# Optimization experiments

Hardware: AMD Instinct MI355X
Metric: run time of the kernel (lower is better)

## Reference

```python
import jax, jax.numpy as jnp
import numpy as np
import math

B, T, C = 4, 2048, 1024
N_HEAD = 16
HEAD_DIM = C // N_HEAD


def setup_inputs() -> dict:
    key = jax.random.key(0)
    k1, k2, k3, k4, k5 = jax.random.split(key, 5)
    s = 1.0 / math.sqrt(C)
    return {
        "x": jax.random.normal(k1, (B, T, C), dtype=jnp.float32),
        "W_attn": jax.random.normal(k2, (3 * C, C), dtype=jnp.float32) * s,
        "b_attn": jax.random.normal(k3, (3 * C,), dtype=jnp.float32) * 0.02,
        "W_proj": jax.random.normal(k4, (C, C), dtype=jnp.float32) * s,
        "b_proj": jax.random.normal(k5, (C,), dtype=jnp.float32) * 0.02,
    }


def reference(x, W_attn, b_attn, W_proj, b_proj):
    Bx, Tx, Cx = x.shape
    # QKV projection (torch Linear: x @ W.T + b), split into q,k,v
    qkv = jnp.einsum("btc,dc->btd", x, W_attn) + b_attn  # [B,T,3C]
    q, k, v = jnp.split(qkv, 3, axis=-1)
    # [B,T,C] -> [B,H,T,hd]
    def to_heads(t):
        return t.reshape(Bx, Tx, N_HEAD, HEAD_DIM).transpose(0, 2, 1, 3)
    q, k, v = to_heads(q), to_heads(k), to_heads(v)
    scale = 1.0 / math.sqrt(HEAD_DIM)
    att = jnp.einsum("bhqd,bhkd->bhqk", q, k) * scale  # [B,H,T,T]
    causal = jnp.tril(jnp.ones((Tx, Tx), dtype=bool))
    att = jnp.where(causal, att, -jnp.inf)
    att = jax.nn.softmax(att, axis=-1)
    y = jnp.einsum("bhqk,bhkd->bhqd", att, v)  # [B,H,T,hd]
    y = y.transpose(0, 2, 1, 3).reshape(Bx, Tx, Cx)
    y = jnp.einsum("btc,dc->btd", y, W_proj) + b_proj
    return y
```

## Files before the change

kernel.cpp:

```cpp
#include <hip/hip_runtime.h>
#include <hip/hip_bf16.h>
#include <stdint.h>

typedef unsigned short u16;
typedef __attribute__((ext_vector_type(8))) short bf16x8;
typedef __attribute__((ext_vector_type(4))) short s16x4;
typedef __attribute__((ext_vector_type(4))) float f32x4;

#define B_SZ 4
#define T_SZ 2048
#define C_SZ 1024
#define NH   16
#define HD   64
#define LOG2E 1.44269504088896340736f

__device__ __forceinline__ u16 f2bf(float f) {
  unsigned int u = __float_as_uint(f);
  u += 0x7fffu + ((u >> 16) & 1u);
  return (u16)(u >> 16);
}
__device__ __forceinline__ u16 f2bf_hu(float f) {
  return (u16)((__float_as_uint(f) + 0x8000u) >> 16);
}
__device__ __forceinline__ void gload_lds16(const u16* g, u16* l) {
  __builtin_amdgcn_global_load_lds((const __attribute__((address_space(1))) void*)g,
                                   (__attribute__((address_space(3))) void*)l, 16, 0, 0);
}

__global__ void cast_f32_bf16(const float* __restrict__ in, u16* __restrict__ out, int n8) {
  int i = blockIdx.x * blockDim.x + threadIdx.x;
  if (i < n8) {
    const float4* p = (const float4*)in + (size_t)i * 2;
    float4 a = p[0], b = p[1];
    bf16x8 o;
    o[0] = (short)f2bf(a.x); o[1] = (short)f2bf(a.y);
    o[2] = (short)f2bf(a.z); o[3] = (short)f2bf(a.w);
    o[4] = (short)f2bf(b.x); o[5] = (short)f2bf(b.y);
    o[6] = (short)f2bf(b.z); o[7] = (short)f2bf(b.w);
    ((bf16x8*)out)[i] = o;
  }
}

template <int MODE>
__launch_bounds__(256, 3)
__global__ void gemm_bt(const u16* __restrict__ A, const u16* __restrict__ Bw,
                        const float* __restrict__ bias,
                        void* __restrict__ O0, void* __restrict__ O1, void* __restrict__ O2,
                        int M, int N, int K) {
  __shared__ __align__(16) u16 As[128 * 32];
  __shared__ __align__(16) u16 Bs[128 * 32];
  const int tid = threadIdx.x;
  const int lane = tid & 63;
  const int w = tid >> 6;
  const int wr = w >> 1, wc = w & 1;
  const int quad = lane >> 4, l16 = lane & 15;
  const int m0 = blockIdx.y * 128;
  const int n0 = blockIdx.x * 128;

  const int srow = lane >> 2;
  const int scol = (lane & 3) * 8;
  const u16* gA = A + (size_t)(m0 + w * 32 + srow) * K + scol;
  const u16* gB = Bw + (size_t)(n0 + w * 32 + srow) * K + scol;
  u16* lA0 = &As[(w * 32) * 32];
  u16* lA1 = &As[(w * 32 + 16) * 32];
  u16* lB0 = &Bs[(w * 32) * 32];
  u16* lB1 = &Bs[(w * 32 + 16) * 32];
  const size_t rstep = (size_t)16 * K;

  f32x4 acc[4][4];
#pragma unroll
  for (int i = 0; i < 4; i++)
#pragma unroll
    for (int j = 0; j < 4; j++) acc[i][j] = (f32x4){0.f, 0.f, 0.f, 0.f};

  for (int k0 = 0; k0 < K; k0 += 32) {
    __syncthreads();
    gload_lds16(gA + k0, lA0);
    gload_lds16(gA + rstep + k0, lA1);
    gload_lds16(gB + k0, lB0);
    gload_lds16(gB + rstep + k0, lB1);
    __syncthreads();
    bf16x8 af[4], bfr[4];
#pragma unroll
    for (int mt = 0; mt < 4; mt++)
      af[mt] = *(const bf16x8*)&As[(wr * 64 + mt * 16 + l16) * 32 + quad * 8];
#pragma unroll
    for (int nt = 0; nt < 4; nt++)
      bfr[nt] = *(const bf16x8*)&Bs[(wc * 64 + nt * 16 + l16) * 32 + quad * 8];
#pragma unroll
    for (int mt = 0; mt < 4; mt++)
#pragma unroll
      for (int nt = 0; nt < 4; nt++)
        acc[mt][nt] = __builtin_amdgcn_mfma_f32_16x16x32_bf16(af[mt], bfr[nt], acc[mt][nt], 0, 0, 0);
  }

  float bv[4];
#pragma unroll
  for (int nt = 0; nt < 4; nt++) bv[nt] = bias[n0 + wc * 64 + nt * 16 + l16];

  if (MODE == 0) {
    float* Cout = (float*)O0;
#pragma unroll
    for (int mt = 0; mt < 4; mt++) {
      const int row = m0 + wr * 64 + mt * 16 + quad * 4;
#pragma unroll
      for (int nt = 0; nt < 4; nt++) {
        const int col = n0 + wc * 64 + nt * 16 + l16;
#pragma unroll
        for (int r = 0; r < 4; r++)
          Cout[(size_t)(row + r) * N + col] = acc[mt][nt][r] + bv[nt];
      }
    }
  } else {
    const int nsec = (n0 + wc * 64) >> 10;
    const int hh = ((n0 + wc * 64) >> 6) & 15;
    if (nsec < 2) {
      u16* dst = (u16*)(nsec == 0 ? O0 : O1);
#pragma unroll
      for (int mt = 0; mt < 4; mt++) {
        const int row = m0 + wr * 64 + mt * 16 + quad * 4;
        const int bb = row >> 11;
        const int t = row & 2047;
#pragma unroll
        for (int nt = 0; nt < 4; nt++) {
          const int dh = nt * 16 + l16;
          const size_t a = (((size_t)bb * NH + hh) * T_SZ + t) * HD + dh;
#pragma unroll
          for (int r = 0; r < 4; r++)
            dst[a + (size_t)r * HD] = f2bf(acc[mt][nt][r] + bv[nt]);
        }
      }
    } else {
      u16* vth = (u16*)O2;
#pragma unroll
      for (int mt = 0; mt < 4; mt++) {
        const int row = m0 + wr * 64 + mt * 16 + quad * 4;
        const int bb = row >> 11;
        const int t = row & 2047;
#pragma unroll
        for (int nt = 0; nt < 4; nt++) {
          const int dh = nt * 16 + l16;
          s16x4 pk;
#pragma unroll
          for (int r = 0; r < 4; r++) pk[r] = (short)f2bf(acc[mt][nt][r] + bv[nt]);
          *(s16x4*)&vth[(((size_t)bb * NH + hh) * HD + dh) * T_SZ + t] = pk;
        }
      }
    }
  }
}

__device__ __forceinline__ void attn_step(
    int kb, int kbn, int w, int quad, int l16, int qt128, int sw0, int sw1,
    const u16* gK0, const u16* gK1, const u16* gV0, const u16* gV1,
    u16* KsF, u16* VsF, u16* PsW,
    const bf16x8 (&qf)[2][2], f32x4 (&o)[2][4], float (&l_i)[2][4]) {
  __syncthreads();

  if (kb + 1 < kbn) {
    const int nb = (kb + 1) & 1;
    const size_t ko = (size_t)(kb + 1) * 64 * HD;
    const int vo = (kb + 1) * 64;
    gload_lds16(gK0 + ko, KsF + nb * 4096 + (2 * w) * 512);
    gload_lds16(gK1 + ko, KsF + nb * 4096 + (2 * w + 1) * 512);
    gload_lds16(gV0 + vo, VsF + nb * 4096 + (2 * w) * 512);
    gload_lds16(gV1 + vo, VsF + nb * 4096 + (2 * w + 1) * 512);
  }

  const u16* Kb = KsF + (kb & 1) * 4096;
  const u16* Vb = VsF + (kb & 1) * 4096;
  const int kt0 = kb * 64;
  const float SC = 0.125f * LOG2E;

#pragma unroll
  for (int m = 0; m < 2; m++) {
    const int mrow = qt128 + w * 32 + m * 16;
    const int qr = mrow + quad * 4;
    const bool diag = (kt0 + 64 > mrow);

    f32x4 s[4];
    __builtin_amdgcn_s_setprio(1);
#pragma unroll
    for (int nt = 0; nt < 4; nt++) {
      bf16x8 kf0 = *(const bf16x8*)&Kb[(nt * 16 + l16) * 64 + sw0];
      bf16x8 kf1 = *(const bf16x8*)&Kb[(nt * 16 + l16) * 64 + sw1];
      f32x4 t0 = (f32x4){0.f, 0.f, 0.f, 0.f};
      t0 = __builtin_amdgcn_mfma_f32_16x16x32_bf16(qf[m][0], kf0, t0, 0, 0, 0);
      t0 = __builtin_amdgcn_mfma_f32_16x16x32_bf16(qf[m][1], kf1, t0, 0, 0, 0);
      s[nt] = t0;
    }
    __builtin_amdgcn_s_setprio(0);

    if (diag) {
#pragma unroll
      for (int nt = 0; nt < 4; nt++) {
        const int dk = kt0 + nt * 16 + l16 - qr;
#pragma unroll
        for (int r = 0; r < 4; r++) {
          float v = (dk > r) ? -10000.f : s[nt][r] * SC;
          s[nt][r] = exp2f(v);
        }
      }
    } else {
#pragma unroll
      for (int nt = 0; nt < 4; nt++)
#pragma unroll
        for (int r = 0; r < 4; r++)
          s[nt][r] = exp2f(s[nt][r] * SC);
    }
#pragma unroll
    for (int r = 0; r < 4; r++)
      l_i[m][r] += (s[0][r] + s[1][r]) + (s[2][r] + s[3][r]);

#pragma unroll
    for (int nt = 0; nt < 4; nt++)
#pragma unroll
      for (int r = 0; r < 4; r++)
        PsW[(quad * 4 + r) * 72 + nt * 16 + l16] = f2bf_hu(s[nt][r]);
    bf16x8 p0 = *(const bf16x8*)&PsW[l16 * 72 + quad * 8];
    bf16x8 p1 = *(const bf16x8*)&PsW[l16 * 72 + 32 + quad * 8];
    __builtin_amdgcn_s_setprio(1);
#pragma unroll
    for (int nt = 0; nt < 4; nt++) {
      bf16x8 v0 = *(const bf16x8*)&Vb[(nt * 16 + l16) * 64 + sw0];
      bf16x8 v1 = *(const bf16x8*)&Vb[(nt * 16 + l16) * 64 + sw1];
      o[m][nt] = __builtin_amdgcn_mfma_f32_16x16x32_bf16(p0, v0, o[m][nt], 0, 0, 0);
      o[m][nt] = __builtin_amdgcn_mfma_f32_16x16x32_bf16(p1, v1, o[m][nt], 0, 0, 0);
    }
    __builtin_amdgcn_s_setprio(0);
  }
}

__launch_bounds__(256, 3)
__global__ void attn_fused(const u16* __restrict__ qh, const u16* __restrict__ kh,
                           const u16* __restrict__ vth, u16* __restrict__ out) {
  __shared__ __align__(16) u16 Ks[2][64 * 64];
  __shared__ __align__(16) u16 Vs[2][64 * 64];
  __shared__ __align__(16) u16 Ps[4][16 * 72];
  const int qt = 15 - blockIdx.z;
  const int h = blockIdx.x, b = blockIdx.y;
  const int tid = threadIdx.x;
  const int lane = tid & 63, w = tid >> 6;
  const int quad = lane >> 4, l16 = lane & 15;
  const size_t bh = (size_t)b * NH + h;
  const u16* Kbase = kh + bh * T_SZ * HD;
  const u16* Vbase = vth + bh * HD * T_SZ;
  const int qt128 = qt * 128;

  const int dr = lane >> 3;
  const int dc = (lane & 7) ^ dr;
  const u16* gK0 = Kbase + (size_t)(2 * w * 8 + dr) * HD + dc * 8;
  const u16* gK1 = Kbase + (size_t)((2 * w + 1) * 8 + dr) * HD + dc * 8;
  const u16* gV0 = Vbase + (size_t)(2 * w * 8 + dr) * T_SZ + dc * 8;
  const u16* gV1 = Vbase + (size_t)((2 * w + 1) * 8 + dr) * T_SZ + dc * 8;
  u16* KsF = &Ks[0][0];
  u16* VsF = &Vs[0][0];
  u16* PsW = &Ps[w][0];

  bf16x8 qf[2][2];
#pragma unroll
  for (int m = 0; m < 2; m++) {
    const int t = qt128 + w * 32 + m * 16 + l16;
    const u16* qrow = qh + (bh * T_SZ + t) * HD;
    qf[m][0] = *(const bf16x8*)(qrow + quad * 8);
    qf[m][1] = *(const bf16x8*)(qrow + 32 + quad * 8);
  }

  f32x4 o[2][4];
  float l_i[2][4];
#pragma unroll
  for (int m = 0; m < 2; m++)
#pragma unroll
    for (int i = 0; i < 4; i++) {
      o[m][i] = (f32x4){0.f, 0.f, 0.f, 0.f};
      l_i[m][i] = 0.f;
    }

  const int kbn = 2 * qt + 2;
  const int sw0 = (quad ^ (l16 & 7)) * 8;
  const int sw1 = ((4 + quad) ^ (l16 & 7)) * 8;

  gload_lds16(gK0, KsF + (2 * w) * 512);
  gload_lds16(gK1, KsF + (2 * w + 1) * 512);
  gload_lds16(gV0, VsF + (2 * w) * 512);
  gload_lds16(gV1, VsF + (2 * w + 1) * 512);

  for (int kb = 0; kb < kbn; kb++)
    attn_step(kb, kbn, w, quad, l16, qt128, sw0, sw1,
              gK0, gK1, gV0, gV1, KsF, VsF, PsW, qf, o, l_i);

#pragma unroll
  for (int m = 0; m < 2; m++)
#pragma unroll
    for (int r = 0; r < 4; r++) {
      float v = l_i[m][r];
      v += __shfl_xor(v, 1);
      v += __shfl_xor(v, 2);
      v += __shfl_xor(v, 4);
      v += __shfl_xor(v, 8);
      const float inv = 1.f / v;
      const int t = qt128 + w * 32 + m * 16 + quad * 4 + r;
      const size_t orow = ((size_t)b * T_SZ + t) * C_SZ + (size_t)h * HD;
#pragma unroll
      for (int nt = 0; nt < 4; nt++)
        out[orow + nt * 16 + l16] = f2bf(o[m][nt][r] * inv);
    }
}

extern "C" void kernel_launch(void* const* d_in, const int* in_sizes, int n_in,
                              void* d_out, int out_size, void* d_ws, size_t ws_size,
                              hipStream_t stream) {
  (void)in_sizes; (void)n_in; (void)out_size; (void)ws_size;
  const float* x      = (const float*)d_in[0];
  const float* W_attn = (const float*)d_in[1];
  const float* b_attn = (const float*)d_in[2];
  const float* W_proj = (const float*)d_in[3];
  const float* b_proj = (const float*)d_in[4];
  float* out = (float*)d_out;

  char* ws = (char*)d_ws;
  u16* xb  = (u16*)ws;  ws += (size_t)8192 * 1024 * 2;
  u16* Wab = (u16*)ws;  ws += (size_t)3072 * 1024 * 2;
  u16* Wpb = (u16*)ws;  ws += (size_t)1024 * 1024 * 2;
  u16* qhb = (u16*)ws;  ws += (size_t)8192 * 1024 * 2;
  u16* khb = (u16*)ws;  ws += (size_t)8192 * 1024 * 2;
  u16* vtb = (u16*)ws;  ws += (size_t)8192 * 1024 * 2;
  u16* aob = (u16*)ws;

  dim3 blk(256);
  cast_f32_bf16<<<(8192 * 1024 / 8 + 255) / 256, blk, 0, stream>>>(x, xb, 8192 * 1024 / 8);
  cast_f32_bf16<<<(3072 * 1024 / 8 + 255) / 256, blk, 0, stream>>>(W_attn, Wab, 3072 * 1024 / 8);
  cast_f32_bf16<<<(1024 * 1024 / 8 + 255) / 256, blk, 0, stream>>>(W_proj, Wpb, 1024 * 1024 / 8);

  gemm_bt<1><<<dim3(3072 / 128, 8192 / 128), blk, 0, stream>>>(
      xb, Wab, b_attn, qhb, khb, vtb, 8192, 3072, 1024);
  attn_fused<<<dim3(NH, B_SZ, 16), blk, 0, stream>>>(qhb, khb, vtb, aob);
  gemm_bt<0><<<dim3(1024 / 128, 8192 / 128), blk, 0, stream>>>(
      aob, Wpb, b_proj, out, nullptr, nullptr, 8192, 1024, 1024);
}
```

Baseline: 267.7 us.

## Rewrite GEMMs with double-buffered swizzled LDS, fuse casts, fold softmax scale into Q

The two GEMMs get a new kernel body with a K-tile of 64, double-buffered LDS filled by direct global-to-LDS loads, an XOR-swizzled LDS layout, workgroup index swizzling for cache locality, and a V-transpose epilogue staged through LDS so global stores are coalesced. The three cast kernels are merged into one launch. The softmax scale and log2e factor are folded into Q at the QKV epilogue. The attention step is reorganised to share K and V fragment loads across both m-subtiles and skips the fully masked last block for the first two waves. The 64KB dynamic LDS drops occupancy to 2 blocks per CU, and the early return inside a step that contains a barrier could be a synchronisation hazard.

```diff
diff --git a/kernel.cpp b/kernel.cpp
--- a/kernel.cpp
+++ b/kernel.cpp
@@ -27,125 +27,185 @@
                                    (__attribute__((address_space(3))) void*)l, 16, 0, 0);
 }
 
-__global__ void cast_f32_bf16(const float* __restrict__ in, u16* __restrict__ out, int n8) {
+__global__ void cast3_f32_bf16(const float* __restrict__ x, const float* __restrict__ wa,
+                               const float* __restrict__ wp, u16* __restrict__ xb,
+                               u16* __restrict__ wab, u16* __restrict__ wpb) {
+  const int n1 = 8192 * 1024 / 8, n2 = 3072 * 1024 / 8, n3 = 1024 * 1024 / 8;
   int i = blockIdx.x * blockDim.x + threadIdx.x;
-  if (i < n8) {
-    const float4* p = (const float4*)in + (size_t)i * 2;
-    float4 a = p[0], b = p[1];
-    bf16x8 o;
-    o[0] = (short)f2bf(a.x); o[1] = (short)f2bf(a.y);
-    o[2] = (short)f2bf(a.z); o[3] = (short)f2bf(a.w);
-    o[4] = (short)f2bf(b.x); o[5] = (short)f2bf(b.y);
-    o[6] = (short)f2bf(b.z); o[7] = (short)f2bf(b.w);
-    ((bf16x8*)out)[i] = o;
-  }
-}
-
-template <int MODE>
-__launch_bounds__(256, 3)
-__global__ void gemm_bt(const u16* __restrict__ A, const u16* __restrict__ Bw,
-                        const float* __restrict__ bias,
-                        void* __restrict__ O0, void* __restrict__ O1, void* __restrict__ O2,
-                        int M, int N, int K) {
-  __shared__ __align__(16) u16 As[128 * 32];
-  __shared__ __align__(16) u16 Bs[128 * 32];
-  const int tid = threadIdx.x;
-  const int lane = tid & 63;
-  const int w = tid >> 6;
-  const int wr = w >> 1, wc = w & 1;
-  const int quad = lane >> 4, l16 = lane & 15;
-  const int m0 = blockIdx.y * 128;
-  const int n0 = blockIdx.x * 128;
-
-  const int srow = lane >> 2;
-  const int scol = (lane & 3) * 8;
-  const u16* gA = A + (size_t)(m0 + w * 32 + srow) * K + scol;
-  const u16* gB = Bw + (size_t)(n0 + w * 32 + srow) * K + scol;
-  u16* lA0 = &As[(w * 32) * 32];
-  u16* lA1 = &As[(w * 32 + 16) * 32];
-  u16* lB0 = &Bs[(w * 32) * 32];
-  u16* lB1 = &Bs[(w * 32 + 16) * 32];
-  const size_t rstep = (size_t)16 * K;
-
-  f32x4 acc[4][4];
-#pragma unroll
-  for (int i = 0; i < 4; i++)
-#pragma unroll
-    for (int j = 0; j < 4; j++) acc[i][j] = (f32x4){0.f, 0.f, 0.f, 0.f};
-
-  for (int k0 = 0; k0 < K; k0 += 32) {
-    __syncthreads();
-    gload_lds16(gA + k0, lA0);
-    gload_lds16(gA + rstep + k0, lA1);
-    gload_lds16(gB + k0, lB0);
-    gload_lds16(gB + rstep + k0, lB1);
-    __syncthreads();
-    bf16x8 af[4], bfr[4];
-#pragma unroll
-    for (int mt = 0; mt < 4; mt++)
-      af[mt] = *(const bf16x8*)&As[(wr * 64 + mt * 16 + l16) * 32 + quad * 8];
-#pragma unroll
-    for (int nt = 0; nt < 4; nt++)
-      bfr[nt] = *(const bf16x8*)&Bs[(wc * 64 + nt * 16 + l16) * 32 + quad * 8];
-#pragma unroll
-    for (int mt = 0; mt < 4; mt++)
-#pragma unroll
-      for (int nt = 0; nt < 4; nt++)
-        acc[mt][nt] = __builtin_amdgcn_mfma_f32_16x16x32_bf16(af[mt], bfr[nt], acc[mt][nt], 0, 0, 0);
-  }
-
+  const float* in; u16* out; int idx;
+  if (i < n1)            { in = x;  out = xb;  idx = i; }
+  else if (i < n1 + n2)  { in = wa; out = wab; idx = i - n1; }
+  else if (i < n1 + n2 + n3) { in = wp; out = wpb; idx = i - n1 - n2; }
+  else return;
+  const float4* p = (const float4*)in + (size_t)idx * 2;
+  float4 a = p[0], b = p[1];
+  bf16x8 o;
+  o[0] = (short)f2bf(a.x); o[1] = (short)f2bf(a.y);
+  o[2] = (short)f2bf(a.z); o[3] = (short)f2bf(a.w);
+  o[4] = (short)f2bf(b.x); o[5] = (short)f2bf(b.y);
+  o[6] = (short)f2bf(b.z); o[7] = (short)f2bf(b.w);
+  ((bf16x8*)out)[idx] = o;
+}
+
+#define GEMM128_PROLOG(A_, B_)                                                \
+  extern __shared__ u16 lds[];                                                \
+  u16* As = lds;                                         \
+  u16* Bs = lds + 16384;                                 \
+  const int tid = threadIdx.x;                                                \
+  const int lane = tid & 63, w = tid >> 6;                                    \
+  const int wm = w >> 1, wn = w & 1;                                          \
+  const int quad = lane >> 4, l16 = lane & 15;                                \
+  const int gx = gridDim.x;                                                   \
+  const int nwg = gx * gridDim.y;                                             \
+  const int wg0 = blockIdx.y * gx + blockIdx.x;                               \
+  const int swz = (wg0 & 7) * (nwg >> 3) + (wg0 >> 3);                        \
+  const int n0 = (swz % gx) * 128;                                            \
+  const int m0 = (swz / gx) * 128;                                            \
+  const int dr8 = lane >> 3;                                                  \
+  const int dc8 = (lane & 7) ^ dr8;                                           \
+  const u16* gAL = A_ + (size_t)(m0 + w * 32 + dr8) * K + dc8 * 8;            \
+  const u16* gBL = B_ + (size_t)(n0 + w * 32 + dr8) * K + dc8 * 8;            \
+  const int NT = K >> 6;                                                      \
+  auto stageA = [&](int tile) {                                               \
+    u16* d = As + (tile & 1) * 8192 + w * 2048;                               \
+    const u16* g = gAL + (size_t)tile * 64;                                   \
+    _Pragma("unroll")                                                         \
+    for (int sg = 0; sg < 4; ++sg)                                            \
+      gload_lds16(g + (size_t)(sg * 8) * K, d + sg * 512);                    \
+  };                                                                          \
+  auto stageB = [&](int tile) {                                               \
+    u16* d = Bs + (tile & 1) * 8192 + w * 2048;                               \
+    const u16* g = gBL + (size_t)tile * 64;                                   \
+    _Pragma("unroll")                                                         \
+    for (int sg = 0; sg < 4; ++sg)                                            \
+      gload_lds16(g + (size_t)(sg * 8) * K, d + sg * 512);                    \
+  };                                                                          \
+  f32x4 acc[4][4];                                                            \
+  _Pragma("unroll")                                                           \
+  for (int i = 0; i < 4; i++)                                                 \
+    _Pragma("unroll")                                                         \
+    for (int j = 0; j < 4; j++) acc[i][j] = (f32x4){0.f, 0.f, 0.f, 0.f};      \
+  stageA(0); stageB(0);                                                       \
+  asm volatile("s_waitcnt vmcnt(0)" ::: "memory");                            \
+  __builtin_amdgcn_s_barrier();                                               \
+  const int sK0 = ((quad) ^ (l16 & 7)) * 8;                                   \
+  const int sK1 = ((4 + quad) ^ (l16 & 7)) * 8;                               \
+  for (int tile = 0; tile < NT; ++tile) {                                     \
+    const u16* Ab = As + (tile & 1) * 8192;                                   \
+    const u16* Bb = Bs + (tile & 1) * 8192;                                   \
+    _Pragma("unroll")                                                         \
+    for (int mp = 0; mp < 2; ++mp) {                                          \
+      bf16x8 af[2][2], bfr[4][2];                                             \
+      _Pragma("unroll")                                                       \
+      for (int a = 0; a < 2; ++a) {                                           \
+        const int ro = (wm * 64 + (mp * 2 + a) * 16 + l16) * 64;              \
+        af[a][0] = *(const bf16x8*)&Ab[ro + sK0];                             \
+        af[a][1] = *(const bf16x8*)&Ab[ro + sK1];                             \
+      }                                                                       \
+      _Pragma("unroll")                                                       \
+      for (int nt = 0; nt < 4; ++nt) {                                        \
+        const int ro = (wn * 64 + nt * 16 + l16) * 64;                        \
+        bfr[nt][0] = *(const bf16x8*)&Bb[ro + sK0];                           \
+        bfr[nt][1] = *(const bf16x8*)&Bb[ro + sK1];                           \
+      }                                                                       \
+      if (mp == 0 && tile + 1 < NT) { stageA(tile + 1); stageB(tile + 1); }   \
+      asm volatile("s_waitcnt lgkmcnt(8)");                                   \
+      asm volatile("" ::: "memory");                                          \
+      __builtin_amdgcn_s_barrier();                                           \
+      asm volatile("s_waitcnt lgkmcnt(0)" ::: "memory");                      \
+      __builtin_amdgcn_sched_barrier(0);                                      \
+      __builtin_amdgcn_s_setprio(1);                                          \
+      _Pragma("unroll")                                                       \
+      for (int a = 0; a < 2; ++a)                                             \
+        _Pragma("unroll")                                                     \
+        for (int nt = 0; nt < 4; ++nt) {                                      \
+          f32x4 c = acc[mp * 2 + a][nt];                                      \
+          c = __builtin_amdgcn_mfma_f32_16x16x32_bf16(af[a][0], bfr[nt][0], c, 0, 0, 0); \
+          c = __builtin_amdgcn_mfma_f32_16x16x32_bf16(af[a][1], bfr[nt][1], c, 0, 0, 0); \
+          acc[mp * 2 + a][nt] = c;                                            \
+        }                                                                     \
+      __builtin_amdgcn_s_setprio(0);                                          \
+      if (mp == 1) asm volatile("s_waitcnt vmcnt(0)" ::: "memory");           \
+      asm volatile("" ::: "memory");                                          \
+      __builtin_amdgcn_s_barrier();                                           \
+    }                                                                         \
+  }
+
+__launch_bounds__(256, 2)
+__global__ void gemm128_qkv(const u16* __restrict__ A, const u16* __restrict__ Bw,
+                            const float* __restrict__ bias,
+                            u16* __restrict__ O0, u16* __restrict__ O1, u16* __restrict__ O2,
+                            int M, int N, int K) {
+  GEMM128_PROLOG(A, Bw)
+
+  const int ncol = n0 + wn * 64;
   float bv[4];
 #pragma unroll
-  for (int nt = 0; nt < 4; nt++) bv[nt] = bias[n0 + wc * 64 + nt * 16 + l16];
-
-  if (MODE == 0) {
-    float* Cout = (float*)O0;
+  for (int nt = 0; nt < 4; nt++) bv[nt] = bias[ncol + nt * 16 + l16];
+
+  const int nsec = ncol >> 10;
+  const int hh = (ncol >> 6) & 15;
+  if (nsec < 2) {
+    u16* dst = (nsec == 0 ? O0 : O1);
+    const float qs = (nsec == 0) ? (0.125f * LOG2E) : 1.0f;
 #pragma unroll
     for (int mt = 0; mt < 4; mt++) {
-      const int row = m0 + wr * 64 + mt * 16 + quad * 4;
+      const int row = m0 + wm * 64 + mt * 16 + quad * 4;
+      const int bb = row >> 11;
+      const int t = row & 2047;
 #pragma unroll
       for (int nt = 0; nt < 4; nt++) {
-        const int col = n0 + wc * 64 + nt * 16 + l16;
+        const int dh = nt * 16 + l16;
+        const size_t a = (((size_t)bb * NH + hh) * T_SZ + t) * HD + dh;
 #pragma unroll
         for (int r = 0; r < 4; r++)
-          Cout[(size_t)(row + r) * N + col] = acc[mt][nt][r] + bv[nt];
+          dst[a + (size_t)r * HD] = f2bf((acc[mt][nt][r] + bv[nt]) * qs);
       }
     }
   } else {
-    const int nsec = (n0 + wc * 64) >> 10;
-    const int hh = ((n0 + wc * 64) >> 6) & 15;
-    if (nsec < 2) {
-      u16* dst = (u16*)(nsec == 0 ? O0 : O1);
-#pragma unroll
-      for (int mt = 0; mt < 4; mt++) {
-        const int row = m0 + wr * 64 + mt * 16 + quad * 4;
-        const int bb = row >> 11;
-        const int t = row & 2047;
-#pragma unroll
-        for (int nt = 0; nt < 4; nt++) {
-          const int dh = nt * 16 + l16;
-          const size_t a = (((size_t)bb * NH + hh) * T_SZ + t) * HD + dh;
-#pragma unroll
-          for (int r = 0; r < 4; r++)
-            dst[a + (size_t)r * HD] = f2bf(acc[mt][nt][r] + bv[nt]);
-        }
+    u16* vth = O2;
+    u16* S = lds + (size_t)w * (64 * 88);
+#pragma unroll
+    for (int mt = 0; mt < 4; ++mt)
+#pragma unroll
+      for (int nt = 0; nt < 4; ++nt) {
+        s16x4 pk;
+#pragma unroll
+        for (int r = 0; r < 4; ++r) pk[r] = (short)f2bf(acc[mt][nt][r] + bv[nt]);
+        *(s16x4*)&S[(nt * 16 + l16) * 88 + mt * 16 + quad * 4] = pk;
       }
-    } else {
-      u16* vth = (u16*)O2;
-#pragma unroll
-      for (int mt = 0; mt < 4; mt++) {
-        const int row = m0 + wr * 64 + mt * 16 + quad * 4;
-        const int bb = row >> 11;
-        const int t = row & 2047;
-#pragma unroll
-        for (int nt = 0; nt < 4; nt++) {
-          const int dh = nt * 16 + l16;
-          s16x4 pk;
-#pragma unroll
-          for (int r = 0; r < 4; r++) pk[r] = (short)f2bf(acc[mt][nt][r] + bv[nt]);
-          *(s16x4*)&vth[(((size_t)bb * NH + hh) * HD + dh) * T_SZ + t] = pk;
-        }
-      }
+    const int tbase = m0 + wm * 64;
+    const int bb = tbase >> 11;
+    const int tb = tbase & 2047;
+    const size_t vrow = ((size_t)bb * NH + hh) * HD;
+    const int tc = (lane & 7) * 8;
+#pragma unroll
+    for (int i = 0; i < 8; ++i) {
+      const int nr = i * 8 + (lane >> 3);
+      bf16x8 vv = *(const bf16x8*)&S[nr * 88 + tc];
+      *(bf16x8*)&vth[(vrow + nr) * T_SZ + tb + tc] = vv;
+    }
+  }
+}
+
+__launch_bounds__(256, 2)
+__global__ void gemm128_proj(const u16* __restrict__ A, const u16* __restrict__ Bw,
+                             const float* __restrict__ bias, float* __restrict__ Cout,
+                             int M, int N, int K) {
+  GEMM128_PROLOG(A, Bw)
+
+  float bv[4];
+#pragma unroll
+  for (int nt = 0; nt < 4; nt++) bv[nt] = bias[n0 + wn * 64 + nt * 16 + l16];
+#pragma unroll
+  for (int mt = 0; mt < 4; mt++) {
+    const int row = m0 + wm * 64 + mt * 16 + quad * 4;
+#pragma unroll
+    for (int nt = 0; nt < 4; nt++) {
+      const int col = n0 + wn * 64 + nt * 16 + l16;
+#pragma unroll
+      for (int r = 0; r < 4; r++)
+        Cout[(size_t)(row + r) * N + col] = acc[mt][nt][r] + bv[nt];
     }
   }
 }
@@ -167,38 +227,43 @@
     gload_lds16(gV1 + vo, VsF + nb * 4096 + (2 * w + 1) * 512);
   }
 
+  if (kb == kbn - 1 && w < 2) return;
+
   const u16* Kb = KsF + (kb & 1) * 4096;
   const u16* Vb = VsF + (kb & 1) * 4096;
   const int kt0 = kb * 64;
-  const float SC = 0.125f * LOG2E;
-
+
+  f32x4 s[2][4];
+  __builtin_amdgcn_s_setprio(1);
+#pragma unroll
+  for (int nt = 0; nt < 4; nt++) {
+    bf16x8 kf0 = *(const bf16x8*)&Kb[(nt * 16 + l16) * 64 + sw0];
+    bf16x8 kf1 = *(const bf16x8*)&Kb[(nt * 16 + l16) * 64 + sw1];
+#pragma unroll
+    for (int m = 0; m < 2; m++) {
+      f32x4 t0 = (f32x4){0.f, 0.f, 0.f, 0.f};
+      t0 = __builtin_amdgcn_mfma_f32_16x16x32_bf16(qf[m][0], kf0, t0, 0, 0, 0);
+      t0 = __builtin_amdgcn_mfma_f32_16x16x32_bf16(qf[m][1], kf1, t0, 0, 0, 0);
+      s[m][nt] = t0;
+    }
+  }
+  __builtin_amdgcn_s_setprio(0);
+
+  bf16x8 p0a, p1a, p0b, p1b;
 #pragma unroll
   for (int m = 0; m < 2; m++) {
     const int mrow = qt128 + w * 32 + m * 16;
     const int qr = mrow + quad * 4;
     const bool diag = (kt0 + 64 > mrow);
 
-    f32x4 s[4];
-    __builtin_amdgcn_s_setprio(1);
-#pragma unroll
-    for (int nt = 0; nt < 4; nt++) {
-      bf16x8 kf0 = *(const bf16x8*)&Kb[(nt * 16 + l16) * 64 + sw0];
-      bf16x8 kf1 = *(const bf16x8*)&Kb[(nt * 16 + l16) * 64 + sw1];
-      f32x4 t0 = (f32x4){0.f, 0.f, 0.f, 0.f};
-      t0 = __builtin_amdgcn_mfma_f32_16x16x32_bf16(qf[m][0], kf0, t0, 0, 0, 0);
-      t0 = __builtin_amdgcn_mfma_f32_16x16x32_bf16(qf[m][1], kf1, t0, 0, 0, 0);
-      s[nt] = t0;
-    }
-    __builtin_amdgcn_s_setprio(0);
-
     if (diag) {
 #pragma unroll
       for (int nt = 0; nt < 4; nt++) {
         const int dk = kt0 + nt * 16 + l16 - qr;
 #pragma unroll
         for (int r = 0; r < 4; r++) {
-          float v = (dk > r) ? -10000.f : s[nt][r] * SC;
-          s[nt][r] = exp2f(v);
+          float v = (dk > r) ? -10000.f : s[m][nt][r];
+          s[m][nt][r] = exp2f(v);
         }
       }
     } else {
@@ -206,29 +271,37 @@
       for (int nt = 0; nt < 4; nt++)
 #pragma unroll
         for (int r = 0; r < 4; r++)
-          s[nt][r] = exp2f(s[nt][r] * SC);
+          s[m][nt][r] = exp2f(s[m][nt][r]);
     }
 #pragma unroll
     for (int r = 0; r < 4; r++)
-      l_i[m][r] += (s[0][r] + s[1][r]) + (s[2][r] + s[3][r]);
+      l_i[m][r] += (s[m][0][r] + s[m][1][r]) + (s[m][2][r] + s[m][3][r]);
 
 #pragma unroll
     for (int nt = 0; nt < 4; nt++)
 #pragma unroll
       for (int r = 0; r < 4; r++)
-        PsW[(quad * 4 + r) * 72 + nt * 16 + l16] = f2bf_hu(s[nt][r]);
-    bf16x8 p0 = *(const bf16x8*)&PsW[l16 * 72 + quad * 8];
-    bf16x8 p1 = *(const bf16x8*)&PsW[l16 * 72 + 32 + quad * 8];
-    __builtin_amdgcn_s_setprio(1);
-#pragma unroll
-    for (int nt = 0; nt < 4; nt++) {
-      bf16x8 v0 = *(const bf16x8*)&Vb[(nt * 16 + l16) * 64 + sw0];
-      bf16x8 v1 = *(const bf16x8*)&Vb[(nt * 16 + l16) * 64 + sw1];
-      o[m][nt] = __builtin_amdgcn_mfma_f32_16x16x32_bf16(p0, v0, o[m][nt], 0, 0, 0);
-      o[m][nt] = __builtin_amdgcn_mfma_f32_16x16x32_bf16(p1, v1, o[m][nt], 0, 0, 0);
-    }
-    __builtin_amdgcn_s_setprio(0);
-  }
+        PsW[(quad * 4 + r) * 72 + nt * 16 + l16] = f2bf_hu(s[m][nt][r]);
+    if (m == 0) {
+      p0a = *(const bf16x8*)&PsW[l16 * 72 + quad * 8];
+      p1a = *(const bf16x8*)&PsW[l16 * 72 + 32 + quad * 8];
+    } else {
+      p0b = *(const bf16x8*)&PsW[l16 * 72 + quad * 8];
+      p1b = *(const bf16x8*)&PsW[l16 * 72 + 32 + quad * 8];
+    }
+  }
+
+  __builtin_amdgcn_s_setprio(1);
+#pragma unroll
+  for (int nt = 0; nt < 4; nt++) {
+    bf16x8 v0 = *(const bf16x8*)&Vb[(nt * 16 + l16) * 64 + sw0];
+    bf16x8 v1 = *(const bf16x8*)&Vb[(nt * 16 + l16) * 64 + sw1];
+    o[0][nt] = __builtin_amdgcn_mfma_f32_16x16x32_bf16(p0a, v0, o[0][nt], 0, 0, 0);
+    o[0][nt] = __builtin_amdgcn_mfma_f32_16x16x32_bf16(p1a, v1, o[0][nt], 0, 0, 0);
+    o[1][nt] = __builtin_amdgcn_mfma_f32_16x16x32_bf16(p0b, v0, o[1][nt], 0, 0, 0);
+    o[1][nt] = __builtin_amdgcn_mfma_f32_16x16x32_bf16(p1b, v1, o[1][nt], 0, 0, 0);
+  }
+  __builtin_amdgcn_s_setprio(0);
 }
 
 __launch_bounds__(256, 3)
@@ -328,13 +401,11 @@
   u16* aob = (u16*)ws;
 
   dim3 blk(256);
-  cast_f32_bf16<<<(8192 * 1024 / 8 + 255) / 256, blk, 0, stream>>>(x, xb, 8192 * 1024 / 8);
-  cast_f32_bf16<<<(3072 * 1024 / 8 + 255) / 256, blk, 0, stream>>>(W_attn, Wab, 3072 * 1024 / 8);
-  cast_f32_bf16<<<(1024 * 1024 / 8 + 255) / 256, blk, 0, stream>>>(W_proj, Wpb, 1024 * 1024 / 8);
-
-  gemm_bt<1><<<dim3(3072 / 128, 8192 / 128), blk, 0, stream>>>(
+  cast3_f32_bf16<<<6144, blk, 0, stream>>>(x, W_attn, W_proj, xb, Wab, Wpb);
+
+  gemm128_qkv<<<dim3(3072 / 128, 8192 / 128), blk, 65536, stream>>>(
       xb, Wab, b_attn, qhb, khb, vtb, 8192, 3072, 1024);
   attn_fused<<<dim3(NH, B_SZ, 16), blk, 0, stream>>>(qhb, khb, vtb, aob);
-  gemm_bt<0><<<dim3(1024 / 128, 8192 / 128), blk, 0, stream>>>(
-      aob, Wpb, b_proj, out, nullptr, nullptr, 8192, 1024, 1024);
-}
+  gemm128_proj<<<dim3(1024 / 128, 8192 / 128), blk, 65536, stream>>>(
+      aob, Wpb, b_proj, out, 8192, 1024, 1024);
+}
```

Measured after the change: 245.6 us. 1.09x faster.
